# Performance work log

Measured on AMD Instinct MI355X. Metric: run time of the kernel, lower is better.

The kernel has to match this reference:

```python
import math
import jax, jax.numpy as jnp
import numpy as np

EMBED_DIM = 768
NUM_HEADS = 12
HEAD_DIM = EMBED_DIM // NUM_HEADS


def setup_inputs() -> dict:
    key = jax.random.key(0)
    ks = jax.random.split(key, 9)
    R, C, B, E = 128, 512, 1, EMBED_DIM
    x = jax.random.normal(ks[0], (R, C, B, E), dtype=jnp.float32)
    s = 0.02
    # weights stored so that projection is x @ W + b (i.e. torch Linear weight transposed)
    Wq = jax.random.normal(ks[1], (E, E), dtype=jnp.float32) * s
    Wk = jax.random.normal(ks[2], (E, E), dtype=jnp.float32) * s
    Wv = jax.random.normal(ks[3], (E, E), dtype=jnp.float32) * s
    Wo = jax.random.normal(ks[4], (E, E), dtype=jnp.float32) * s
    bq = jnp.zeros((E,), jnp.float32)
    bk = jnp.zeros((E,), jnp.float32)
    bv = jnp.zeros((E,), jnp.float32)
    bo = jnp.zeros((E,), jnp.float32)
    return {"x": x, "Wq": Wq, "bq": bq, "Wk": Wk, "bk": bk,
            "Wv": Wv, "bv": bv, "Wo": Wo, "bo": bo}


def reference(x, Wq, bq, Wk, bk, Wv, bv, Wo, bo):
    R, C, B, E = x.shape
    H, D = NUM_HEADS, HEAD_DIM
    # scaling = head_dim^-0.5 / sqrt(num_rows)  (align_scaling)
    scaling = (D ** -0.5) / math.sqrt(R)
    q = (x @ Wq + bq).reshape(R, C, B, H, D) * scaling
    k = (x @ Wk + bk).reshape(R, C, B, H, D)
    v = (x @ Wv + bv).reshape(R, C, B, H, D)
    # sum attention logits over rows r -> shared [h, n, i, j] attention map
    attn_weights = jnp.einsum('rinhd,rjnhd->hnij', q, k)
    attn_probs = jax.nn.softmax(attn_weights, axis=-1)
    context = jnp.einsum('hnij,rjnhd->rinhd', attn_probs, v)
    context = context.reshape(R, C, B, E)
    output = context @ Wo + bo
    return output, attn_probs
```

## Files before the change

kernel.cpp:

```cpp
#include <hip/hip_runtime.h>
#include <math.h>

#define RDIM 128
#define CDIM 512
#define EDIM 768
#define HDIM 12
#define DDIM 64
#define MDIM (RDIM*CDIM)
#define OUT_ELEMS ((size_t)MDIM*EDIM)
#define HSTRIDE ((size_t)CDIM*RDIM*DDIM)
#define WELEMS (EDIM*EDIM)

typedef unsigned short ushort_t;
typedef __attribute__((ext_vector_type(8))) short bf16x8;
typedef __attribute__((ext_vector_type(8))) unsigned short u16x8;
typedef __attribute__((ext_vector_type(4))) float f32x4;

__device__ __forceinline__ ushort_t f2bf(float f) {
    unsigned u = __float_as_uint(f);
    unsigned r = u + 0x7fffu + ((u >> 16) & 1u);
    return (ushort_t)(r >> 16);
}

__device__ __forceinline__ void gload16(const void* g, void* l) {
    __builtin_amdgcn_global_load_lds(
        (const __attribute__((address_space(1))) unsigned int*)g,
        (__attribute__((address_space(3))) unsigned int*)l, 16, 0, 0);
}

__global__ __launch_bounds__(256)
void cast_x(const float* __restrict__ x, ushort_t* __restrict__ xb) {
    size_t i = ((size_t)blockIdx.x * 256 + threadIdx.x) * 8;
    float4 a = *(const float4*)&x[i];
    float4 b = *(const float4*)&x[i + 4];
    u16x8 o;
    o[0]=f2bf(a.x); o[1]=f2bf(a.y); o[2]=f2bf(a.z); o[3]=f2bf(a.w);
    o[4]=f2bf(b.x); o[5]=f2bf(b.y); o[6]=f2bf(b.z); o[7]=f2bf(b.w);
    *(u16x8*)&xb[i] = o;
}

__global__ __launch_bounds__(256)
void transpose_cast_w(const float* __restrict__ W, ushort_t* __restrict__ Wt) {
    __shared__ ushort_t t[64][66];
    const int k0 = blockIdx.x * 64, n0 = blockIdx.y * 64;
    const int tx = threadIdx.x & 15, ty = threadIdx.x >> 4;
    #pragma unroll
    for (int rep = 0; rep < 4; ++rep) {
        int k = ty + rep * 16;
        float4 v = *(const float4*)&W[(size_t)(k0 + k) * EDIM + n0 + tx*4];
        t[k][tx*4+0] = f2bf(v.x); t[k][tx*4+1] = f2bf(v.y);
        t[k][tx*4+2] = f2bf(v.z); t[k][tx*4+3] = f2bf(v.w);
    }
    __syncthreads();
    #pragma unroll
    for (int rep = 0; rep < 4; ++rep) {
        int n = ty + rep * 16;
        ushort4 o = { t[tx*4+0][n], t[tx*4+1][n], t[tx*4+2][n], t[tx*4+3][n] };
        *(ushort4*)&Wt[(size_t)(n0 + n) * EDIM + k0 + tx*4] = o;
    }
}

__global__ __launch_bounds__(256)
void concat_bias(const float* __restrict__ bq, const float* __restrict__ bk,
                 const float* __restrict__ bv, float* __restrict__ bqkv) {
    int i = blockIdx.x * 256 + threadIdx.x;
    if (i < 768)        bqkv[i] = bq[i];
    else if (i < 1536)  bqkv[i] = bk[i - 768];
    else if (i < 2304)  bqkv[i] = bv[i - 1536];
}

#define SBAR do { __builtin_amdgcn_sched_barrier(0); \
                  __builtin_amdgcn_s_barrier(); \
                  __builtin_amdgcn_sched_barrier(0); } while(0)
#define SCHED0 __builtin_amdgcn_sched_barrier(0)
#define VMCNT(n_) asm volatile("s_waitcnt vmcnt(" #n_ ")" ::: "memory")

template<int M, int N, int K, int LDK, int MODE, int NWG>
__global__ __launch_bounds__(512, 2)
void gemm8(const ushort_t* __restrict__ A, const ushort_t* __restrict__ B,
           const float* __restrict__ bias, float scale,
           float* __restrict__ outF, ushort_t* __restrict__ outB,
           size_t sAh, size_t sBh) {
    __shared__ __align__(16) char smem[131072];
    constexpr int NT = K / 64;

    const int tid = threadIdx.x;
    const int lane = tid & 63, wid = tid >> 6;
    const int wr = wid >> 2, wc = wid & 3;
    const int fr = lane & 15, fs = lane >> 4;
    const int sw = (fr & 7) << 3;

    const int bid = blockIdx.x;
    const int w = (bid & 7) * (NWG / 8) + (bid >> 3);
    int bm, bn, h = 0, ksub = 0, plane = 0, ntile = 0;
    if (MODE == 4)      { ntile = w % 9; bm = (w / 9) * 256; bn = ntile * 256; }
    else if (MODE == 2) { plane = w >> 2; h = plane >> 3; ksub = plane & 7;
                          bm = ((w >> 1) & 1) * 256; bn = (w & 1) * 256; }
    else if (MODE == 3) { h = w >> 6; bm = ((w >> 5) & 1) * 256; bn = (w & 31) * 256; }
    else                { bm = (w / 3) * 256; bn = (w % 3) * 256; }

    const ushort_t* Ab = A + (MODE == 2 || MODE == 3 ? (size_t)h * sAh : 0)
                       + (MODE == 2 ? (size_t)ksub * K : 0) + (size_t)bm * LDK;
    const ushort_t* Bb = B + (MODE == 2 || MODE == 3 ? (size_t)h * sBh : 0)
                       + (MODE == 2 ? (size_t)ksub * K : 0) + (size_t)bn * LDK;

    const int r0 = tid >> 3, s0 = tid & 7;
    const size_t gO0 = (size_t)r0 * LDK + ((s0 ^ (r0 & 7)) * 8);
    const size_t gO1 = gO0 + (size_t)64 * LDK;
    const int l0 = tid * 16, l1 = tid * 16 + 8192;

#define STAGE_A(t_, h_) do { \
    char* d_ = smem + ((((t_) & 1) * 2 + (h_)) * 16384); \
    const ushort_t* s_ = Ab + (size_t)((h_) * 128) * LDK + (t_) * 64; \
    gload16(s_ + gO0, d_ + l0); gload16(s_ + gO1, d_ + l1); } while(0)
#define STAGE_B(t_, h_) do { \
    char* d_ = smem + 65536 + ((((t_) & 1) * 2 + (h_)) * 16384); \
    const ushort_t* s_ = Bb + (size_t)((h_) * 128) * LDK + (t_) * 64; \
    gload16(s_ + gO0, d_ + l0); gload16(s_ + gO1, d_ + l1); } while(0)

    f32x4 acc[8][4];
    #pragma unroll
    for (int i = 0; i < 8; ++i)
        #pragma unroll
        for (int j = 0; j < 4; ++j) acc[i][j] = (f32x4){0.f, 0.f, 0.f, 0.f};
    bf16x8 a_[4][2], a2_[4][2], bb0_[2][2], bb1_[2][2];

#define DSA(t_, mq_, A_) do { \
    const ushort_t* As_ = (const ushort_t*)(smem + ((((t_) & 1) * 2 + wr) * 16384)); \
    _Pragma("unroll") for (int f = 0; f < 4; ++f) \
      _Pragma("unroll") for (int kk = 0; kk < 2; ++kk) \
        A_[f][kk] = *(const bf16x8*)&As_[((mq_) * 64 + f * 16 + fr) * 64 \
                                          + ((kk * 32 + fs * 8) ^ sw)]; } while(0)

#define DSB(t_, nq_, B_) do { \
    const ushort_t* Bs_ = (const ushort_t*)(smem + 65536 + ((((t_) & 1) * 2 + (wc >> 1)) * 16384)); \
    _Pragma("unroll") for (int nf = 0; nf < 2; ++nf) \
      _Pragma("unroll") for (int kk = 0; kk < 2; ++kk) \
        B_[nf][kk] = *(const bf16x8*)&Bs_[((wc & 1) * 64 + (nq_) * 32 + nf * 16 + fr) * 64 \
                                           + ((kk * 32 + fs * 8) ^ sw)]; } while(0)

#define MFMA8(mq_, nq_, B_) do { \
    __builtin_amdgcn_s_setprio(1); \
    _Pragma("unroll") for (int f = 0; f < 4; ++f) \
      _Pragma("unroll") for (int nf2 = 0; nf2 < 2; ++nf2) \
        _Pragma("unroll") for (int kk = 0; kk < 2; ++kk) \
          acc[(mq_) * 4 + f][(nq_) * 2 + nf2] = __builtin_amdgcn_mfma_f32_16x16x32_bf16( \
              a_[f][kk], B_[nf2][kk], acc[(mq_) * 4 + f][(nq_) * 2 + nf2], 0, 0, 0); \
    __builtin_amdgcn_s_setprio(0); } while(0)

#define MFMA8b(mq_, nq_, B_) do { \
    __builtin_amdgcn_s_setprio(1); \
    _Pragma("unroll") for (int f = 0; f < 4; ++f) \
      _Pragma("unroll") for (int nf2 = 0; nf2 < 2; ++nf2) \
        _Pragma("unroll") for (int kk = 0; kk < 2; ++kk) \
          acc[(mq_) * 4 + f][(nq_) * 2 + nf2] = __builtin_amdgcn_mfma_f32_16x16x32_bf16( \
              a2_[f][kk], B_[nf2][kk], acc[(mq_) * 4 + f][(nq_) * 2 + nf2], 0, 0, 0); \
    __builtin_amdgcn_s_setprio(0); } while(0)

    STAGE_B(0, 0); SCHED0;
    STAGE_B(0, 1); SCHED0;
    STAGE_A(0, 0); SCHED0;
    STAGE_A(0, 1); SCHED0;
    VMCNT(0);
    SBAR;

    for (int t = 0; t < NT; ++t) {
        if (t + 1 < NT) {
            STAGE_B(t + 1, 0); STAGE_B(t + 1, 1);
            STAGE_A(t + 1, 0); STAGE_A(t + 1, 1);
        }
        SCHED0;
        DSA(t, 0, a_);  DSB(t, 0, bb0_);
        DSB(t, 1, bb1_);
        DSA(t, 1, a2_);
        MFMA8(0, 0, bb0_);
        MFMA8(0, 1, bb1_);
        MFMA8b(1, 0, bb0_);
        MFMA8b(1, 1, bb1_);
        SCHED0;
        VMCNT(0);
        SBAR;
    }

    if (MODE == 4) {
        const int which = ntile / 3;
        const int hcb = (ntile % 3) * 256;
        if (which < 2) {
            ushort_t* dst = outB + (size_t)which * OUT_ELEMS;
            const float sc = (which == 0) ? scale : 1.f;
            #pragma unroll
            for (int mf = 0; mf < 8; ++mf) {
                #pragma unroll
                for (int nf = 0; nf < 4; ++nf) {
                    const int hcol = hcb + wc*64 + nf*16 + fr;
                    const float bv = bias[which*768 + hcol];
                    const int hh = hcol >> 6, d = hcol & 63;
                    #pragma unroll
                    for (int j = 0; j < 4; ++j) {
                        const int m = bm + wr*128 + mf*16 + fs*4 + j;
                        float v = (acc[mf][nf][j] + bv) * sc;
                        size_t addr = (size_t)hh * HSTRIDE
                                    + (size_t)(m & 511) * 8192 + (m >> 9) * 64 + d;
                        dst[addr] = f2bf(v);
                    }
                }
            }
        } else {
            ushort_t* Ts = (ushort_t*)smem;
            ushort_t* dst = outB + 2 * OUT_ELEMS;
            const int rblk = bm >> 9, jb = bm & 511;
            __syncthreads();
            #pragma unroll
            for (int q = 0; q < 2; ++q) {
                if ((wc >> 1) == q) {
                    #pragma unroll
                    for (int mf = 0; mf < 8; ++mf) {
                        #pragma unroll
                        for (int nf = 0; nf < 4; ++nf) {
                            const int nl = wc*64 + nf*16 + fr;
                            const float bv = bias[1536 + hcb + nl];
                            #pragma unroll
                            for (int j = 0; j < 4; ++j)
                                Ts[(nl & 127)*264 + wr*128 + mf*16 + fs*4 + j] =
                                    f2bf(acc[mf][nf][j] + bv);
                        }
                    }
                }
                __syncthreads();
                #pragma unroll
                for (int it = 0; it < 8; ++it) {
                    const int idx = it * 512 + tid;
                    const int row = idx >> 5, c8 = (idx & 31) * 8;
                    const int nl = q*128 + row;
                    const int hh = (hcb + nl) >> 6, d = nl & 63;
                    uint4 wv;
                    wv.x = *(const uint*)&Ts[row*264 + c8];
                    wv.y = *(const uint*)&Ts[row*264 + c8 + 2];
                    wv.z = *(const uint*)&Ts[row*264 + c8 + 4];
                    wv.w = *(const uint*)&Ts[row*264 + c8 + 6];
                    size_t addr = (size_t)hh * HSTRIDE
                                + (size_t)(rblk*64 + d) * CDIM + jb + c8;
                    *(uint4*)&dst[addr] = wv;
                }
                __syncthreads();
            }
        }
        return;
    }

    #pragma unroll
    for (int mf = 0; mf < 8; ++mf) {
        #pragma unroll
        for (int nf = 0; nf < 4; ++nf) {
            const int n = bn + wc*64 + nf*16 + fr;
            float bv = (MODE == 1) ? bias[n] : 0.f;
            #pragma unroll
            for (int j = 0; j < 4; ++j) {
                const int m = bm + wr*128 + mf*16 + fs*4 + j;
                float v = acc[mf][nf][j];
                if (MODE == 1) {
                    outF[(size_t)m * N + n] = v + bv;
                } else if (MODE == 2) {
                    outF[(size_t)plane * (CDIM*CDIM) + (size_t)m * CDIM + n] = v;
                } else {
                    size_t addr = ((size_t)(n >> 6) * CDIM + m) * EDIM
                                + h * DDIM + (n & 63);
                    outB[addr] = f2bf(v);
                }
            }
        }
    }
}

__global__ __launch_bounds__(256)
void softmax_reduce(const float* __restrict__ part, float* __restrict__ attn,
                    ushort_t* __restrict__ Pb) {
    const int row = blockIdx.x;
    const int h = row >> 9, c = row & 511;
    const int tid = threadIdx.x;
    const int lane = tid & 63, wid = tid >> 6;
    __shared__ float red[8];

    float v0 = 0.f, v1 = 0.f;
    #pragma unroll
    for (int s = 0; s < 8; ++s) {
        const float* p = part + ((size_t)(h*8 + s) * (CDIM*CDIM)) + (size_t)c * CDIM;
        v0 += p[tid];
        v1 += p[tid + 256];
    }
    float m = fmaxf(v0, v1);
    #pragma unroll
    for (int off = 32; off > 0; off >>= 1) m = fmaxf(m, __shfl_down(m, off));
    if (lane == 0) red[wid] = m;
    __syncthreads();
    if (tid == 0) red[4] = fmaxf(fmaxf(red[0], red[1]), fmaxf(red[2], red[3]));
    __syncthreads();
    const float M = red[4];

    float e0 = expf(v0 - M), e1 = expf(v1 - M);
    float s = e0 + e1;
    #pragma unroll
    for (int off = 32; off > 0; off >>= 1) s += __shfl_down(s, off);
    __syncthreads();
    if (lane == 0) red[wid] = s;
    __syncthreads();
    if (tid == 0) red[5] = red[0] + red[1] + red[2] + red[3];
    __syncthreads();
    const float inv = 1.f / red[5];
    float o0 = e0 * inv, o1 = e1 * inv;
    float* pout = attn + (size_t)row * CDIM;
    ushort_t* pb = Pb + (size_t)row * CDIM;
    pout[tid] = o0;        pout[tid + 256] = o1;
    pb[tid]   = f2bf(o0);  pb[tid + 256]   = f2bf(o1);
}

extern "C" void kernel_launch(void* const* d_in, const int* in_sizes, int n_in,
                              void* d_out, int out_size, void* d_ws, size_t ws_size,
                              hipStream_t stream) {
    const float* x  = (const float*)d_in[0];
    const float* Wq = (const float*)d_in[1];
    const float* bq = (const float*)d_in[2];
    const float* Wk = (const float*)d_in[3];
    const float* bk = (const float*)d_in[4];
    const float* Wv = (const float*)d_in[5];
    const float* bv = (const float*)d_in[6];
    const float* Wo = (const float*)d_in[7];
    const float* bo = (const float*)d_in[8];

    float* out   = (float*)d_out;
    float* attnp = out + OUT_ELEMS;

    ushort_t* ws   = (ushort_t*)d_ws;
    ushort_t* xb   = ws;
    ushort_t* Wqkv = xb + OUT_ELEMS;
    ushort_t* Wto  = Wqkv + 3*WELEMS;
    float*    bqkv = (float*)(Wto + WELEMS);
    ushort_t* Qp   = Wto + WELEMS + 4608;
    ushort_t* Kp   = Qp + OUT_ELEMS;
    ushort_t* Vt   = Kp + OUT_ELEMS;
    ushort_t* Pb   = Vt + OUT_ELEMS;
    float*    part = (float*)xb;
    ushort_t* ctxb = xb;

    const float scaling = 0.011048543456039806f;

    cast_x<<<MDIM*EDIM/(256*8), 256, 0, stream>>>(x, xb);
    dim3 wt(EDIM/64, EDIM/64);
    transpose_cast_w<<<wt, 256, 0, stream>>>(Wq, Wqkv);
    transpose_cast_w<<<wt, 256, 0, stream>>>(Wk, Wqkv + WELEMS);
    transpose_cast_w<<<wt, 256, 0, stream>>>(Wv, Wqkv + 2*WELEMS);
    transpose_cast_w<<<wt, 256, 0, stream>>>(Wo, Wto);
    concat_bias<<<9, 256, 0, stream>>>(bq, bk, bv, bqkv);

    gemm8<MDIM, 2304, EDIM, EDIM, 4, 2304><<<2304, 512, 0, stream>>>(
        xb, Wqkv, bqkv, scaling, nullptr, Qp, 0, 0);

    gemm8<CDIM, CDIM, 1024, 8192, 2, 384><<<384, 512, 0, stream>>>(
        Qp, Kp, nullptr, 1.f, part, nullptr, HSTRIDE, HSTRIDE);

    softmax_reduce<<<HDIM*CDIM, 256, 0, stream>>>(part, attnp, Pb);

    gemm8<CDIM, 8192, CDIM, CDIM, 3, 768><<<768, 512, 0, stream>>>(
        Pb, Vt, nullptr, 1.f, nullptr, ctxb, (size_t)CDIM*CDIM, HSTRIDE);

    gemm8<MDIM, EDIM, EDIM, EDIM, 1, 768><<<768, 512, 0, stream>>>(
        ctxb, Wto, bo, 1.f, out, nullptr, 0, 0);
}
```

Baseline: 603.9 us.

## Split GEMM 256x256 tile across 16 waves with 64x64 per-wave subtiles

Renames gemm8 to gemm16 and launches every GEMM with 1024 threads instead of 512. Each of the 16 waves now computes a 64x64 sub-tile instead of 128x64, which halves the accumulator registers and gives one global load per thread per stage. The aim is more resident waves to hide memory and LDS latency. In exchange, LDS fragment reads per MFMA go up. `__launch_bounds__(1024, 4)` may also squeeze the per-thread register budget enough to cause spills.

```diff
diff --git a/kernel.cpp b/kernel.cpp
--- a/kernel.cpp
+++ b/kernel.cpp
@@ -76,11 +76,11 @@
 #define VMCNT(n_) asm volatile("s_waitcnt vmcnt(" #n_ ")" ::: "memory")
 
 template<int M, int N, int K, int LDK, int MODE, int NWG>
-__global__ __launch_bounds__(512, 2)
-void gemm8(const ushort_t* __restrict__ A, const ushort_t* __restrict__ B,
-           const float* __restrict__ bias, float scale,
-           float* __restrict__ outF, ushort_t* __restrict__ outB,
-           size_t sAh, size_t sBh) {
+__global__ __launch_bounds__(1024, 4)
+void gemm16(const ushort_t* __restrict__ A, const ushort_t* __restrict__ B,
+            const float* __restrict__ bias, float scale,
+            float* __restrict__ outF, ushort_t* __restrict__ outB,
+            size_t sAh, size_t sBh) {
     __shared__ __align__(16) char smem[131072];
     constexpr int NT = K / 64;
 
@@ -106,55 +106,45 @@
 
     const int r0 = tid >> 3, s0 = tid & 7;
     const size_t gO0 = (size_t)r0 * LDK + ((s0 ^ (r0 & 7)) * 8);
-    const size_t gO1 = gO0 + (size_t)64 * LDK;
-    const int l0 = tid * 16, l1 = tid * 16 + 8192;
+    const int l0 = tid * 16;
 
 #define STAGE_A(t_, h_) do { \
     char* d_ = smem + ((((t_) & 1) * 2 + (h_)) * 16384); \
     const ushort_t* s_ = Ab + (size_t)((h_) * 128) * LDK + (t_) * 64; \
-    gload16(s_ + gO0, d_ + l0); gload16(s_ + gO1, d_ + l1); } while(0)
+    gload16(s_ + gO0, d_ + l0); } while(0)
 #define STAGE_B(t_, h_) do { \
     char* d_ = smem + 65536 + ((((t_) & 1) * 2 + (h_)) * 16384); \
     const ushort_t* s_ = Bb + (size_t)((h_) * 128) * LDK + (t_) * 64; \
-    gload16(s_ + gO0, d_ + l0); gload16(s_ + gO1, d_ + l1); } while(0)
-
-    f32x4 acc[8][4];
-    #pragma unroll
-    for (int i = 0; i < 8; ++i)
+    gload16(s_ + gO0, d_ + l0); } while(0)
+
+    f32x4 acc[4][4];
+    #pragma unroll
+    for (int i = 0; i < 4; ++i)
         #pragma unroll
         for (int j = 0; j < 4; ++j) acc[i][j] = (f32x4){0.f, 0.f, 0.f, 0.f};
-    bf16x8 a_[4][2], a2_[4][2], bb0_[2][2], bb1_[2][2];
-
-#define DSA(t_, mq_, A_) do { \
-    const ushort_t* As_ = (const ushort_t*)(smem + ((((t_) & 1) * 2 + wr) * 16384)); \
+    bf16x8 a_[4][2], b_[4][2];
+
+#define DSA(t_) do { \
+    const ushort_t* As_ = (const ushort_t*)(smem + ((((t_) & 1) * 2 + (wr >> 1)) * 16384)); \
     _Pragma("unroll") for (int f = 0; f < 4; ++f) \
       _Pragma("unroll") for (int kk = 0; kk < 2; ++kk) \
-        A_[f][kk] = *(const bf16x8*)&As_[((mq_) * 64 + f * 16 + fr) * 64 \
+        a_[f][kk] = *(const bf16x8*)&As_[((wr & 1) * 64 + f * 16 + fr) * 64 \
                                           + ((kk * 32 + fs * 8) ^ sw)]; } while(0)
 
-#define DSB(t_, nq_, B_) do { \
+#define DSB(t_) do { \
     const ushort_t* Bs_ = (const ushort_t*)(smem + 65536 + ((((t_) & 1) * 2 + (wc >> 1)) * 16384)); \
-    _Pragma("unroll") for (int nf = 0; nf < 2; ++nf) \
+    _Pragma("unroll") for (int nf = 0; nf < 4; ++nf) \
       _Pragma("unroll") for (int kk = 0; kk < 2; ++kk) \
-        B_[nf][kk] = *(const bf16x8*)&Bs_[((wc & 1) * 64 + (nq_) * 32 + nf * 16 + fr) * 64 \
+        b_[nf][kk] = *(const bf16x8*)&Bs_[((wc & 1) * 64 + nf * 16 + fr) * 64 \
                                            + ((kk * 32 + fs * 8) ^ sw)]; } while(0)
 
-#define MFMA8(mq_, nq_, B_) do { \
+#define MFMA32 do { \
     __builtin_amdgcn_s_setprio(1); \
     _Pragma("unroll") for (int f = 0; f < 4; ++f) \
-      _Pragma("unroll") for (int nf2 = 0; nf2 < 2; ++nf2) \
+      _Pragma("unroll") for (int nf = 0; nf < 4; ++nf) \
         _Pragma("unroll") for (int kk = 0; kk < 2; ++kk) \
-          acc[(mq_) * 4 + f][(nq_) * 2 + nf2] = __builtin_amdgcn_mfma_f32_16x16x32_bf16( \
-              a_[f][kk], B_[nf2][kk], acc[(mq_) * 4 + f][(nq_) * 2 + nf2], 0, 0, 0); \
-    __builtin_amdgcn_s_setprio(0); } while(0)
-
-#define MFMA8b(mq_, nq_, B_) do { \
-    __builtin_amdgcn_s_setprio(1); \
-    _Pragma("unroll") for (int f = 0; f < 4; ++f) \
-      _Pragma("unroll") for (int nf2 = 0; nf2 < 2; ++nf2) \
-        _Pragma("unroll") for (int kk = 0; kk < 2; ++kk) \
-          acc[(mq_) * 4 + f][(nq_) * 2 + nf2] = __builtin_amdgcn_mfma_f32_16x16x32_bf16( \
-              a2_[f][kk], B_[nf2][kk], acc[(mq_) * 4 + f][(nq_) * 2 + nf2], 0, 0, 0); \
+          acc[f][nf] = __builtin_amdgcn_mfma_f32_16x16x32_bf16( \
+              a_[f][kk], b_[nf][kk], acc[f][nf], 0, 0, 0); \
     __builtin_amdgcn_s_setprio(0); } while(0)
 
     STAGE_B(0, 0); SCHED0;
@@ -170,13 +160,8 @@
             STAGE_A(t + 1, 0); STAGE_A(t + 1, 1);
         }
         SCHED0;
-        DSA(t, 0, a_);  DSB(t, 0, bb0_);
-        DSB(t, 1, bb1_);
-        DSA(t, 1, a2_);
-        MFMA8(0, 0, bb0_);
-        MFMA8(0, 1, bb1_);
-        MFMA8b(1, 0, bb0_);
-        MFMA8b(1, 1, bb1_);
+        DSA(t); DSB(t);
+        MFMA32;
         SCHED0;
         VMCNT(0);
         SBAR;
@@ -189,7 +174,7 @@
             ushort_t* dst = outB + (size_t)which * OUT_ELEMS;
             const float sc = (which == 0) ? scale : 1.f;
             #pragma unroll
-            for (int mf = 0; mf < 8; ++mf) {
+            for (int f = 0; f < 4; ++f) {
                 #pragma unroll
                 for (int nf = 0; nf < 4; ++nf) {
                     const int hcol = hcb + wc*64 + nf*16 + fr;
@@ -197,8 +182,8 @@
                     const int hh = hcol >> 6, d = hcol & 63;
                     #pragma unroll
                     for (int j = 0; j < 4; ++j) {
-                        const int m = bm + wr*128 + mf*16 + fs*4 + j;
-                        float v = (acc[mf][nf][j] + bv) * sc;
+                        const int m = bm + wr*64 + f*16 + fs*4 + j;
+                        float v = (acc[f][nf][j] + bv) * sc;
                         size_t addr = (size_t)hh * HSTRIDE
                                     + (size_t)(m & 511) * 8192 + (m >> 9) * 64 + d;
                         dst[addr] = f2bf(v);
@@ -214,22 +199,22 @@
             for (int q = 0; q < 2; ++q) {
                 if ((wc >> 1) == q) {
                     #pragma unroll
-                    for (int mf = 0; mf < 8; ++mf) {
+                    for (int f = 0; f < 4; ++f) {
                         #pragma unroll
                         for (int nf = 0; nf < 4; ++nf) {
                             const int nl = wc*64 + nf*16 + fr;
                             const float bv = bias[1536 + hcb + nl];
                             #pragma unroll
                             for (int j = 0; j < 4; ++j)
-                                Ts[(nl & 127)*264 + wr*128 + mf*16 + fs*4 + j] =
-                                    f2bf(acc[mf][nf][j] + bv);
+                                Ts[(nl & 127)*264 + wr*64 + f*16 + fs*4 + j] =
+                                    f2bf(acc[f][nf][j] + bv);
                         }
                     }
                 }
                 __syncthreads();
                 #pragma unroll
-                for (int it = 0; it < 8; ++it) {
-                    const int idx = it * 512 + tid;
+                for (int it = 0; it < 4; ++it) {
+                    const int idx = it * 1024 + tid;
                     const int row = idx >> 5, c8 = (idx & 31) * 8;
                     const int nl = q*128 + row;
                     const int hh = (hcb + nl) >> 6, d = nl & 63;
@@ -249,15 +234,15 @@
     }
 
     #pragma unroll
-    for (int mf = 0; mf < 8; ++mf) {
+    for (int f = 0; f < 4; ++f) {
         #pragma unroll
         for (int nf = 0; nf < 4; ++nf) {
             const int n = bn + wc*64 + nf*16 + fr;
             float bv = (MODE == 1) ? bias[n] : 0.f;
             #pragma unroll
             for (int j = 0; j < 4; ++j) {
-                const int m = bm + wr*128 + mf*16 + fs*4 + j;
-                float v = acc[mf][nf][j];
+                const int m = bm + wr*64 + f*16 + fs*4 + j;
+                float v = acc[f][nf][j];
                 if (MODE == 1) {
                     outF[(size_t)m * N + n] = v + bv;
                 } else if (MODE == 2) {
@@ -352,17 +337,17 @@
     transpose_cast_w<<<wt, 256, 0, stream>>>(Wo, Wto);
     concat_bias<<<9, 256, 0, stream>>>(bq, bk, bv, bqkv);
 
-    gemm8<MDIM, 2304, EDIM, EDIM, 4, 2304><<<2304, 512, 0, stream>>>(
+    gemm16<MDIM, 2304, EDIM, EDIM, 4, 2304><<<2304, 1024, 0, stream>>>(
         xb, Wqkv, bqkv, scaling, nullptr, Qp, 0, 0);
 
-    gemm8<CDIM, CDIM, 1024, 8192, 2, 384><<<384, 512, 0, stream>>>(
+    gemm16<CDIM, CDIM, 1024, 8192, 2, 384><<<384, 1024, 0, stream>>>(
         Qp, Kp, nullptr, 1.f, part, nullptr, HSTRIDE, HSTRIDE);
 
     softmax_reduce<<<HDIM*CDIM, 256, 0, stream>>>(part, attnp, Pb);
 
-    gemm8<CDIM, 8192, CDIM, CDIM, 3, 768><<<768, 512, 0, stream>>>(
+    gemm16<CDIM, 8192, CDIM, CDIM, 3, 768><<<768, 1024, 0, stream>>>(
         Pb, Vt, nullptr, 1.f, nullptr, ctxb, (size_t)CDIM*CDIM, HSTRIDE);
 
-    gemm8<MDIM, EDIM, EDIM, EDIM, 1, 768><<<768, 512, 0, stream>>>(
+    gemm16<MDIM, EDIM, EDIM, EDIM, 1, 768><<<768, 1024, 0, stream>>>(
         ctxb, Wto, bo, 1.f, out, nullptr, 0, 0);
 }
```

After: 1.250 ms. 2.07x slower.
